# Optimization experiments

Hardware: AMD Instinct MI355X
Metric: run time of the kernel (lower is better)

The kernel has to match this reference:

```python
import jax, jax.numpy as jnp
import numpy as np

N = 50000   # nodes
E = 800000  # edges (avg degree 16)
D = 128     # in = hidden = out feats


def setup_inputs() -> dict:
    key = jax.random.key(0)
    ks = jax.random.split(key, 9)
    x = jax.random.normal(ks[0], (N, D), dtype=jnp.float32)
    edge_index = jax.random.randint(ks[1], (2, E), 0, N, dtype=jnp.int64)
    s = 1.0 / np.sqrt(D)
    # SAGEConv layer 0 (128 -> 128): lin_l (aggregated neighbors, with bias), lin_r (root, no bias)
    Wl0 = jax.random.uniform(ks[2], (D, D), jnp.float32, -s, s)
    Wr0 = jax.random.uniform(ks[3], (D, D), jnp.float32, -s, s)
    b0 = jax.random.uniform(ks[4], (D,), jnp.float32, -s, s)
    # SAGEConv layer 1 (128 -> 128)
    Wl1 = jax.random.uniform(ks[5], (D, D), jnp.float32, -s, s)
    Wr1 = jax.random.uniform(ks[6], (D, D), jnp.float32, -s, s)
    b1 = jax.random.uniform(ks[7], (D,), jnp.float32, -s, s)
    return {"x": x, "edge_index": edge_index,
            "Wl0": Wl0, "Wr0": Wr0, "b0": b0,
            "Wl1": Wl1, "Wr1": Wr1, "b1": b1}


def _sage_conv(x, src, dst, Wl, Wr, b):
    # mean aggregation of neighbor messages x[src] into dst nodes
    msgs = x[src]                                                    # [E, D]
    summed = jax.ops.segment_sum(msgs, dst, num_segments=N)         # [N, D]
    deg = jax.ops.segment_sum(jnp.ones((src.shape[0], 1), x.dtype), dst,
                              num_segments=N)                       # [N, 1]
    agg = summed / jnp.maximum(deg, 1.0)
    # out = lin_l(agg) + lin_r(x); only lin_l has bias (PyG default)
    return agg @ Wl.T + b + x @ Wr.T


def reference(x, edge_index, Wl0, Wr0, b0, Wl1, Wr1, b1):
    src, dst = edge_index[0], edge_index[1]
    h = jax.nn.relu(_sage_conv(x, src, dst, Wl0, Wr0, b0))
    out = _sage_conv(h, src, dst, Wl1, Wr1, b1)  # no ReLU on last layer
    return out
```

## Files before the change

### kernel.cpp

```cpp
#include <hip/hip_runtime.h>


#define D 128
#define NBITS 7
#define BNODES 128
#define GA 64
typedef unsigned short u16;
typedef unsigned u32;
typedef short bf16x8 __attribute__((ext_vector_type(8)));
typedef float f32x4 __attribute__((ext_vector_type(4)));

__device__ __forceinline__ u16 f2bf(float f) {
    union { float f; unsigned u; } x;
    x.f = f;
    unsigned r = x.u + 0x7FFF + ((x.u >> 16) & 1);
    return (u16)(r >> 16);
}
__device__ __forceinline__ float bf2f(u16 b) {
    union { unsigned u; float f; } x;
    x.u = ((unsigned)b) << 16;
    return x.f;
}

__global__ __launch_bounds__(1024) void hist_and_convert(
        const int* __restrict__ dst, int* __restrict__ Gcounts, int E, int NB, int chunk,
        const float* __restrict__ x, u16* __restrict__ xb, int xQuads,
        const float* __restrict__ w0, const float* __restrict__ w1,
        const float* __restrict__ w2, const float* __restrict__ w3,
        u16* __restrict__ o0, u16* __restrict__ o1,
        u16* __restrict__ o2, u16* __restrict__ o3) {
    if (blockIdx.x < GA) {
        __shared__ int cnt[512];
        for (int i = threadIdx.x; i < NB; i += 1024) cnt[i] = 0;
        __syncthreads();
        int base = blockIdx.x * chunk;
        int end = base + chunk; if (end > E) end = E;
        for (int e = base + threadIdx.x; e < end; e += 1024)
            atomicAdd(&cnt[dst[e] >> NBITS], 1);
        __syncthreads();
        for (int b = threadIdx.x; b < NB; b += 1024)
            Gcounts[b * GA + blockIdx.x] = cnt[b];
    } else {
        int i = (blockIdx.x - GA) * 1024 + threadIdx.x;
        if (i < xQuads) {
            float4 v = *(const float4*)&x[i * 4];
            ushort4 o;
            o.x = f2bf(v.x); o.y = f2bf(v.y); o.z = f2bf(v.z); o.w = f2bf(v.w);
            *(ushort4*)&xb[i * 4] = o;
        } else {
            int j = i - xQuads;
            const int q = D * D / 4;
            if (j < 4 * q) {
                int m = j / q, k = j % q;
                const float* in = (m == 0) ? w0 : (m == 1) ? w1 : (m == 2) ? w2 : w3;
                u16* op = (m == 0) ? o0 : (m == 1) ? o1 : (m == 2) ? o2 : o3;
                float4 v = *(const float4*)&in[k * 4];
                ushort4 o;
                o.x = f2bf(v.x); o.y = f2bf(v.y); o.z = f2bf(v.z); o.w = f2bf(v.w);
                *(ushort4*)&op[k * 4] = o;
            }
        }
    }
}

__global__ __launch_bounds__(1024) void scan1_kernel(const int* __restrict__ in,
                                                     int* __restrict__ excl,
                                                     int* __restrict__ totals, int n) {
    int chunk = blockIdx.x;
    int i = chunk * 1024 + threadIdx.x;
    int v = (i < n) ? in[i] : 0;
    int lane = threadIdx.x & 63;
    int wid = threadIdx.x >> 6;
    int s = v;
    #pragma unroll
    for (int off = 1; off < 64; off <<= 1) {
        int t = __shfl_up(s, off);
        if (lane >= off) s += t;
    }
    __shared__ int wsum[16];
    if (lane == 63) wsum[wid] = s;
    __syncthreads();
    if (wid == 0) {
        int ws = (lane < 16) ? wsum[lane] : 0;
        #pragma unroll
        for (int off = 1; off < 16; off <<= 1) {
            int t = __shfl_up(ws, off);
            if (lane >= off) ws += t;
        }
        if (lane < 16) wsum[lane] = ws;
    }
    __syncthreads();
    int wave_off = (wid > 0) ? wsum[wid - 1] : 0;
    int incl = s + wave_off;
    if (i < n) excl[i] = incl - v;
    if (threadIdx.x == 1023) totals[chunk] = incl;
}

__device__ __forceinline__ void load_choff(const int* __restrict__ totals,
                                           int nChunks, int* choff) {
    if (threadIdx.x < 64) {
        int t = threadIdx.x;
        int v = (t < nChunks) ? totals[t] : 0;
        int s = v;
        #pragma unroll
        for (int off = 1; off < 64; off <<= 1) {
            int u = __shfl_up(s, off);
            if (t >= off) s += u;
        }
        if (t < 32) choff[t] = s - v;
    }
}

__global__ __launch_bounds__(1024) void bucket_scatter(const int* __restrict__ src,
                                                       const int* __restrict__ dst,
                                                       const int* __restrict__ excl,
                                                       const int* __restrict__ totals,
                                                       u32* __restrict__ Ebuck,
                                                       int E, int NB, int chunk, int nChunks) {
    __shared__ int cur[512];
    __shared__ int choff[32];
    load_choff(totals, nChunks, choff);
    __syncthreads();
    for (int b = threadIdx.x; b < NB; b += 1024) {
        int idx = b * GA + blockIdx.x;
        cur[b] = excl[idx] + choff[idx >> 10];
    }
    __syncthreads();
    int base = blockIdx.x * chunk;
    int end = base + chunk; if (end > E) end = E;
    for (int e = base + threadIdx.x; e < end; e += 1024) {
        int d = dst[e];
        int b = d >> NBITS;
        int pos = atomicAdd(&cur[b], 1);
        Ebuck[pos] = ((u32)(d & (BNODES - 1)) << 16) | (u32)src[e];
    }
}

__global__ __launch_bounds__(256) void bucket_sort_csr(const u32* __restrict__ Ebuck,
                                                       const int* __restrict__ excl_g,
                                                       const int* __restrict__ totals,
                                                       int* __restrict__ row_ptr,
                                                       u16* __restrict__ csr,
                                                       int E, int N, int NB, int nChunks) {
    __shared__ int hist[BNODES], excl[BNODES], cur[BNODES];
    __shared__ u16 sorted[8192];
    __shared__ int choff[32];
    load_choff(totals, nChunks, choff);
    __syncthreads();
    int b = blockIdx.x;
    int idx0 = b * GA;
    int start = excl_g[idx0] + choff[idx0 >> 10];
    int endv = E;
    if (b + 1 < NB) {
        int idx1 = (b + 1) * GA;
        endv = excl_g[idx1] + choff[idx1 >> 10];
    }
    int cnt = endv - start;
    if (cnt > 8192) cnt = 8192;
    for (int i = threadIdx.x; i < BNODES; i += 256) hist[i] = 0;
    __syncthreads();
    for (int i = threadIdx.x; i < cnt; i += 256)
        atomicAdd(&hist[Ebuck[start + i] >> 16], 1);
    __syncthreads();
    if (threadIdx.x == 0) {
        int run = 0;
        for (int i = 0; i < BNODES; ++i) { excl[i] = run; run += hist[i]; }
    }
    __syncthreads();
    for (int i = threadIdx.x; i < BNODES; i += 256) {
        cur[i] = excl[i];
        int g = b * BNODES + i;
        if (g <= N) row_ptr[g] = start + excl[i];
    }
    __syncthreads();
    for (int i = threadIdx.x; i < cnt; i += 256) {
        u32 r = Ebuck[start + i];
        int pos = atomicAdd(&cur[r >> 16], 1);
        sorted[pos] = (u16)(r & 0xFFFF);
    }
    __syncthreads();
    for (int i = threadIdx.x; i < cnt; i += 256)
        csr[start + i] = sorted[i];
}

__global__ __launch_bounds__(256) void aggregate_bf16(const u16* __restrict__ xb,
                                                      const int* __restrict__ row_ptr,
                                                      const u16* __restrict__ csr,
                                                      u16* __restrict__ aggb, int n) {
    int node = blockIdx.x * 4 + (threadIdx.x >> 6);
    if (node >= n) return;
    int lane = threadIdx.x & 63;
    int half = lane >> 5;
    int fl = (lane & 31) * 4;
    int begin = row_ptr[node], end = row_ptr[node + 1];
    float a0 = 0.f, a1 = 0.f, a2 = 0.f, a3 = 0.f;
    int j = begin + half;
    for (; j + 2 < end; j += 4) {
        int s0 = csr[j], s1 = csr[j + 2];
        ushort4 v0 = *(const ushort4*)&xb[s0 * D + fl];
        ushort4 v1 = *(const ushort4*)&xb[s1 * D + fl];
        a0 += bf2f(v0.x) + bf2f(v1.x);
        a1 += bf2f(v0.y) + bf2f(v1.y);
        a2 += bf2f(v0.z) + bf2f(v1.z);
        a3 += bf2f(v0.w) + bf2f(v1.w);
    }
    if (j < end) {
        int s0 = csr[j];
        ushort4 v0 = *(const ushort4*)&xb[s0 * D + fl];
        a0 += bf2f(v0.x); a1 += bf2f(v0.y); a2 += bf2f(v0.z); a3 += bf2f(v0.w);
    }
    a0 += __shfl_xor(a0, 32);
    a1 += __shfl_xor(a1, 32);
    a2 += __shfl_xor(a2, 32);
    a3 += __shfl_xor(a3, 32);
    if (half == 0) {
        int d = end - begin;
        if (d < 1) d = 1;
        float inv = 1.0f / (float)d;
        ushort4 o;
        o.x = f2bf(a0 * inv); o.y = f2bf(a1 * inv);
        o.z = f2bf(a2 * inv); o.w = f2bf(a3 * inv);
        *(ushort4*)&aggb[node * D + fl] = o;
    }
}

#define LSTR 136

__global__ __launch_bounds__(256) void gemm_mfma(const u16* __restrict__ Aroot,
                                                 const u16* __restrict__ Wr,
                                                 const u16* __restrict__ Agg,
                                                 const u16* __restrict__ Wl,
                                                 const float* __restrict__ bias,
                                                 void* __restrict__ out,
                                                 int n, int mode) {
    __shared__ __align__(16) u16 Lr[64 * LSTR];
    __shared__ __align__(16) u16 Lg[64 * LSTR];
    const int tid = threadIdx.x;
    const int n0 = blockIdx.x * 64;

    {
        int row = tid >> 4;
        int c = (tid & 15) * 8;
        #pragma unroll
        for (int p = 0; p < 4; ++p) {
            int r = p * 16 + row;
            int g = n0 + r;
            float4 vr = make_float4(0.f, 0.f, 0.f, 0.f);
            float4 vg = make_float4(0.f, 0.f, 0.f, 0.f);
            if (g < n) {
                vr = *(const float4*)&Aroot[g * D + c];
                vg = *(const float4*)&Agg[g * D + c];
            }
            *(float4*)&Lr[r * LSTR + c] = vr;
            *(float4*)&Lg[r * LSTR + c] = vg;
        }
    }

    const int wave = tid >> 6;
    const int lane = tid & 63;
    const int quad = lane >> 4;
    const int l16 = lane & 15;

    bf16x8 wr[2][4], wl[2][4];
    #pragma unroll
    for (int mt = 0; mt < 2; ++mt) {
        int jrow = wave * 32 + mt * 16 + l16;
        #pragma unroll
        for (int kb = 0; kb < 4; ++kb) {
            wr[mt][kb] = *(const bf16x8*)&Wr[jrow * D + kb * 32 + quad * 8];
            wl[mt][kb] = *(const bf16x8*)&Wl[jrow * D + kb * 32 + quad * 8];
        }
    }

    __syncthreads();

    f32x4 acc[4][2];
    #pragma unroll
    for (int it = 0; it < 4; ++it)
        #pragma unroll
        for (int mt = 0; mt < 2; ++mt)
            acc[it][mt] = (f32x4){0.f, 0.f, 0.f, 0.f};

    #pragma unroll
    for (int it = 0; it < 4; ++it) {
        int base = (it * 16 + l16) * LSTR + quad * 8;
        #pragma unroll
        for (int kb = 0; kb < 4; ++kb) {
            bf16x8 bx = *(const bf16x8*)&Lr[base + kb * 32];
            bf16x8 bg = *(const bf16x8*)&Lg[base + kb * 32];
            #pragma unroll
            for (int mt = 0; mt < 2; ++mt) {
                acc[it][mt] = __builtin_amdgcn_mfma_f32_16x16x32_bf16(wr[mt][kb], bx, acc[it][mt], 0, 0, 0);
                acc[it][mt] = __builtin_amdgcn_mfma_f32_16x16x32_bf16(wl[mt][kb], bg, acc[it][mt], 0, 0, 0);
            }
        }
    }

    #pragma unroll
    for (int it = 0; it < 4; ++it) {
        int i = n0 + it * 16 + l16;
        if (i < n) {
            #pragma unroll
            for (int mt = 0; mt < 2; ++mt) {
                int j0 = wave * 32 + mt * 16 + quad * 4;
                float4 bv = *(const float4*)&bias[j0];
                float o0 = acc[it][mt][0] + bv.x;
                float o1 = acc[it][mt][1] + bv.y;
                float o2 = acc[it][mt][2] + bv.z;
                float o3 = acc[it][mt][3] + bv.w;
                if (mode) {
                    o0 = fmaxf(o0, 0.f); o1 = fmaxf(o1, 0.f);
                    o2 = fmaxf(o2, 0.f); o3 = fmaxf(o3, 0.f);
                    ushort4 ob;
                    ob.x = f2bf(o0); ob.y = f2bf(o1); ob.z = f2bf(o2); ob.w = f2bf(o3);
                    *(ushort4*)&((u16*)out)[i * D + j0] = ob;
                } else {
                    float4 of = make_float4(o0, o1, o2, o3);
                    *(float4*)&((float*)out)[i * D + j0] = of;
                }
            }
        }
    }
}


extern "C" void kernel_launch(void* const* d_in, const int* in_sizes, int n_in,
                              void* d_out, int out_size, void* d_ws, size_t ws_size,
                              hipStream_t stream) {
    const float* x = (const float*)d_in[0];
    const int* edge = (const int*)d_in[1];
    const float* Wl0 = (const float*)d_in[2];
    const float* Wr0 = (const float*)d_in[3];
    const float* b0 = (const float*)d_in[4];
    const float* Wl1 = (const float*)d_in[5];
    const float* Wr1 = (const float*)d_in[6];
    const float* b1 = (const float*)d_in[7];

    const int N = in_sizes[0] / D;
    const int E = in_sizes[1] / 2;
    const int* src = edge;
    const int* dst = edge + E;

    char* ws = (char*)d_ws;
    size_t off = 0;
    auto alloc = [&](size_t bytes) {
        char* p = ws + off;
        off += (bytes + 255) & ~(size_t)255;
        return p;
    };
    int* row_ptr = (int*)alloc((size_t)(N + 1) * 4);
    u32* Ebuck = (u32*)alloc((size_t)E * 4);
    u16* csrb = (u16*)alloc((size_t)E * 2);
    u16* xb = (u16*)alloc((size_t)N * D * 2);
    u16* hb = (u16*)alloc((size_t)N * D * 2);
    u16* aggb = (u16*)alloc((size_t)N * D * 2);
    u16* Wl0b = (u16*)alloc((size_t)D * D * 2);
    u16* Wr0b = (u16*)alloc((size_t)D * D * 2);
    u16* Wl1b = (u16*)alloc((size_t)D * D * 2);
    u16* Wr1b = (u16*)alloc((size_t)D * D * 2);
    const int NB = (N + BNODES - 1) / BNODES;
    const int scanN = NB * GA;
    int* Gcounts = (int*)alloc((size_t)scanN * 4);
    int* Sc = (int*)alloc((size_t)scanN * 4);
    int* totals = (int*)alloc(32 * 4);

    (void)ws_size; (void)n_in; (void)out_size;

    const int chunk = (E + GA - 1) / GA;
    const int xQuads = N * D / 4;
    const int convQuads = xQuads + 4 * D * D / 4;
    const int histGrid = GA + (convQuads + 1023) / 1024;
    const int nChunks = (scanN + 1023) / 1024;
    const int aggBlocks = (N + 3) / 4;
    const int gemmBlocks = (N + 63) / 64;

    hist_and_convert<<<histGrid, 1024, 0, stream>>>(
        dst, Gcounts, E, NB, chunk,
        x, xb, xQuads,
        Wl0, Wr0, Wl1, Wr1, Wl0b, Wr0b, Wl1b, Wr1b);
    scan1_kernel<<<nChunks, 1024, 0, stream>>>(Gcounts, Sc, totals, scanN);
    bucket_scatter<<<GA, 1024, 0, stream>>>(src, dst, Sc, totals, Ebuck, E, NB, chunk, nChunks);
    bucket_sort_csr<<<NB, 256, 0, stream>>>(Ebuck, Sc, totals, row_ptr, csrb, E, N, NB, nChunks);

    aggregate_bf16<<<aggBlocks, 256, 0, stream>>>(xb, row_ptr, csrb, aggb, N);
    gemm_mfma<<<gemmBlocks, 256, 0, stream>>>(xb, Wr0b, aggb, Wl0b, b0, hb, N, 1);
    aggregate_bf16<<<aggBlocks, 256, 0, stream>>>(hb, row_ptr, csrb, aggb, N);
    gemm_mfma<<<gemmBlocks, 256, 0, stream>>>(hb, Wr1b, aggb, Wl1b, b1, d_out, N, 0);
}
```

Baseline: 218.9 us.

## Store bf16 features in 32-wide column slabs for cache-local aggregation

Features, hidden activations and aggregates are stored as four slabs of 32 columns each instead of row-major 128 columns. Aggregation processes one slab per group of blocks so the gathered working set is a quarter of the full feature matrix and fits better in cache. In exchange the CSR indices and row pointers are read four times and each gather fetches only 64 bytes per row. The conversion kernel and GEMM loads and stores are adapted to the new layout.

```diff
diff --git a/kernel.cpp b/kernel.cpp
--- a/kernel.cpp
+++ b/kernel.cpp
@@ -24,7 +24,7 @@
 
 __global__ __launch_bounds__(1024) void hist_and_convert(
         const int* __restrict__ dst, int* __restrict__ Gcounts, int E, int NB, int chunk,
-        const float* __restrict__ x, u16* __restrict__ xb, int xQuads,
+        const float* __restrict__ x, u16* __restrict__ xq, int xOcts, int n32,
         const float* __restrict__ w0, const float* __restrict__ w1,
         const float* __restrict__ w2, const float* __restrict__ w3,
         u16* __restrict__ o0, u16* __restrict__ o1,
@@ -42,13 +42,20 @@
             Gcounts[b * GA + blockIdx.x] = cnt[b];
     } else {
         int i = (blockIdx.x - GA) * 1024 + threadIdx.x;
-        if (i < xQuads) {
-            float4 v = *(const float4*)&x[i * 4];
-            ushort4 o;
-            o.x = f2bf(v.x); o.y = f2bf(v.y); o.z = f2bf(v.z); o.w = f2bf(v.w);
-            *(ushort4*)&xb[i * 4] = o;
+        if (i < xOcts) {
+            int node = i >> 4;
+            int f = (i & 15) * 8;
+            int q = f >> 5, off = f & 31;
+            float4 va = *(const float4*)&x[node * D + f];
+            float4 vb = *(const float4*)&x[node * D + f + 4];
+            bf16x8 o;
+            o[0] = (short)f2bf(va.x); o[1] = (short)f2bf(va.y);
+            o[2] = (short)f2bf(va.z); o[3] = (short)f2bf(va.w);
+            o[4] = (short)f2bf(vb.x); o[5] = (short)f2bf(vb.y);
+            o[6] = (short)f2bf(vb.z); o[7] = (short)f2bf(vb.w);
+            *(bf16x8*)&xq[q * n32 + node * 32 + off] = o;
         } else {
-            int j = i - xQuads;
+            int j = i - xOcts;
             const int q = D * D / 4;
             if (j < 4 * q) {
                 int m = j / q, k = j % q;
@@ -183,44 +190,42 @@
         csr[start + i] = sorted[i];
 }
 
-__global__ __launch_bounds__(256) void aggregate_bf16(const u16* __restrict__ xb,
-                                                      const int* __restrict__ row_ptr,
-                                                      const u16* __restrict__ csr,
-                                                      u16* __restrict__ aggb, int n) {
-    int node = blockIdx.x * 4 + (threadIdx.x >> 6);
+__global__ __launch_bounds__(256) void aggregate_q(const u16* __restrict__ xq,
+                                                   const int* __restrict__ row_ptr,
+                                                   const u16* __restrict__ csr,
+                                                   u16* __restrict__ aggq,
+                                                   int n, int nb4, int n32) {
+    int bq = blockIdx.x / nb4;
+    int node = (blockIdx.x % nb4) * 4 + (threadIdx.x >> 6);
     if (node >= n) return;
     int lane = threadIdx.x & 63;
-    int half = lane >> 5;
-    int fl = (lane & 31) * 4;
+    int part = lane >> 4;
+    int fl = (lane & 15) * 2;
+    const u16* base = xq + bq * n32;
     int begin = row_ptr[node], end = row_ptr[node + 1];
-    float a0 = 0.f, a1 = 0.f, a2 = 0.f, a3 = 0.f;
-    int j = begin + half;
-    for (; j + 2 < end; j += 4) {
-        int s0 = csr[j], s1 = csr[j + 2];
-        ushort4 v0 = *(const ushort4*)&xb[s0 * D + fl];
-        ushort4 v1 = *(const ushort4*)&xb[s1 * D + fl];
-        a0 += bf2f(v0.x) + bf2f(v1.x);
-        a1 += bf2f(v0.y) + bf2f(v1.y);
-        a2 += bf2f(v0.z) + bf2f(v1.z);
-        a3 += bf2f(v0.w) + bf2f(v1.w);
-    }
-    if (j < end) {
+    float a0 = 0.f, a1 = 0.f;
+    int j = begin + part;
+    for (; j + 4 < end; j += 8) {
+        int s0 = csr[j], s1 = csr[j + 4];
+        u32 v0 = *(const u32*)&base[s0 * 32 + fl];
+        u32 v1 = *(const u32*)&base[s1 * 32 + fl];
+        a0 += bf2f((u16)v0) + bf2f((u16)v1);
+        a1 += bf2f((u16)(v0 >> 16)) + bf2f((u16)(v1 >> 16));
+    }
+    for (; j < end; j += 4) {
         int s0 = csr[j];
-        ushort4 v0 = *(const ushort4*)&xb[s0 * D + fl];
-        a0 += bf2f(v0.x); a1 += bf2f(v0.y); a2 += bf2f(v0.z); a3 += bf2f(v0.w);
-    }
-    a0 += __shfl_xor(a0, 32);
-    a1 += __shfl_xor(a1, 32);
-    a2 += __shfl_xor(a2, 32);
-    a3 += __shfl_xor(a3, 32);
-    if (half == 0) {
+        u32 v0 = *(const u32*)&base[s0 * 32 + fl];
+        a0 += bf2f((u16)v0);
+        a1 += bf2f((u16)(v0 >> 16));
+    }
+    a0 += __shfl_xor(a0, 16); a0 += __shfl_xor(a0, 32);
+    a1 += __shfl_xor(a1, 16); a1 += __shfl_xor(a1, 32);
+    if (part == 0) {
         int d = end - begin;
         if (d < 1) d = 1;
         float inv = 1.0f / (float)d;
-        ushort4 o;
-        o.x = f2bf(a0 * inv); o.y = f2bf(a1 * inv);
-        o.z = f2bf(a2 * inv); o.w = f2bf(a3 * inv);
-        *(ushort4*)&aggb[node * D + fl] = o;
+        u32 o = (u32)f2bf(a0 * inv) | ((u32)f2bf(a1 * inv) << 16);
+        *(u32*)&aggq[bq * n32 + node * 32 + fl] = o;
     }
 }
 
@@ -232,7 +237,7 @@
                                                  const u16* __restrict__ Wl,
                                                  const float* __restrict__ bias,
                                                  void* __restrict__ out,
-                                                 int n, int mode) {
+                                                 int n, int n32, int mode) {
     __shared__ __align__(16) u16 Lr[64 * LSTR];
     __shared__ __align__(16) u16 Lg[64 * LSTR];
     const int tid = threadIdx.x;
@@ -241,6 +246,9 @@
     {
         int row = tid >> 4;
         int c = (tid & 15) * 8;
+        int q = c >> 5, off = c & 31;
+        const u16* ar = Aroot + q * n32;
+        const u16* ag = Agg + q * n32;
         #pragma unroll
         for (int p = 0; p < 4; ++p) {
             int r = p * 16 + row;
@@ -248,8 +256,8 @@
             float4 vr = make_float4(0.f, 0.f, 0.f, 0.f);
             float4 vg = make_float4(0.f, 0.f, 0.f, 0.f);
             if (g < n) {
-                vr = *(const float4*)&Aroot[g * D + c];
-                vg = *(const float4*)&Agg[g * D + c];
+                vr = *(const float4*)&ar[g * 32 + off];
+                vg = *(const float4*)&ag[g * 32 + off];
             }
             *(float4*)&Lr[r * LSTR + c] = vr;
             *(float4*)&Lg[r * LSTR + c] = vg;
@@ -313,7 +321,8 @@
                     o2 = fmaxf(o2, 0.f); o3 = fmaxf(o3, 0.f);
                     ushort4 ob;
                     ob.x = f2bf(o0); ob.y = f2bf(o1); ob.z = f2bf(o2); ob.w = f2bf(o3);
-                    *(ushort4*)&((u16*)out)[i * D + j0] = ob;
+                    int jj = mt * 16 + quad * 4;
+                    *(ushort4*)&((u16*)out)[wave * n32 + i * 32 + jj] = ob;
                 } else {
                     float4 of = make_float4(o0, o1, o2, o3);
                     *(float4*)&((float*)out)[i * D + j0] = of;
@@ -351,9 +360,9 @@
     int* row_ptr = (int*)alloc((size_t)(N + 1) * 4);
     u32* Ebuck = (u32*)alloc((size_t)E * 4);
     u16* csrb = (u16*)alloc((size_t)E * 2);
-    u16* xb = (u16*)alloc((size_t)N * D * 2);
-    u16* hb = (u16*)alloc((size_t)N * D * 2);
-    u16* aggb = (u16*)alloc((size_t)N * D * 2);
+    u16* xq = (u16*)alloc((size_t)N * D * 2);
+    u16* hq = (u16*)alloc((size_t)N * D * 2);
+    u16* aggq = (u16*)alloc((size_t)N * D * 2);
     u16* Wl0b = (u16*)alloc((size_t)D * D * 2);
     u16* Wr0b = (u16*)alloc((size_t)D * D * 2);
     u16* Wl1b = (u16*)alloc((size_t)D * D * 2);
@@ -367,23 +376,25 @@
     (void)ws_size; (void)n_in; (void)out_size;
 
     const int chunk = (E + GA - 1) / GA;
-    const int xQuads = N * D / 4;
-    const int convQuads = xQuads + 4 * D * D / 4;
-    const int histGrid = GA + (convQuads + 1023) / 1024;
+    const int n32 = N * 32;
+    const int xOcts = N * D / 8;
+    const int convThreads = xOcts + 4 * D * D / 4;
+    const int histGrid = GA + (convThreads + 1023) / 1024;
     const int nChunks = (scanN + 1023) / 1024;
-    const int aggBlocks = (N + 3) / 4;
+    const int nb4 = (N + 3) / 4;
+    const int aggBlocks = 4 * nb4;
     const int gemmBlocks = (N + 63) / 64;
 
     hist_and_convert<<<histGrid, 1024, 0, stream>>>(
         dst, Gcounts, E, NB, chunk,
-        x, xb, xQuads,
+        x, xq, xOcts, n32,
         Wl0, Wr0, Wl1, Wr1, Wl0b, Wr0b, Wl1b, Wr1b);
     scan1_kernel<<<nChunks, 1024, 0, stream>>>(Gcounts, Sc, totals, scanN);
     bucket_scatter<<<GA, 1024, 0, stream>>>(src, dst, Sc, totals, Ebuck, E, NB, chunk, nChunks);
     bucket_sort_csr<<<NB, 256, 0, stream>>>(Ebuck, Sc, totals, row_ptr, csrb, E, N, NB, nChunks);
 
-    aggregate_bf16<<<aggBlocks, 256, 0, stream>>>(xb, row_ptr, csrb, aggb, N);
-    gemm_mfma<<<gemmBlocks, 256, 0, stream>>>(xb, Wr0b, aggb, Wl0b, b0, hb, N, 1);
-    aggregate_bf16<<<aggBlocks, 256, 0, stream>>>(hb, row_ptr, csrb, aggb, N);
-    gemm_mfma<<<gemmBlocks, 256, 0, stream>>>(hb, Wr1b, aggb, Wl1b, b1, d_out, N, 0);
-}
+    aggregate_q<<<aggBlocks, 256, 0, stream>>>(xq, row_ptr, csrb, aggq, N, nb4, n32);
+    gemm_mfma<<<gemmBlocks, 256, 0, stream>>>(xq, Wr0b, aggq, Wl0b, b0, hq, N, n32, 1);
+    aggregate_q<<<aggBlocks, 256, 0, stream>>>(hq, row_ptr, csrb, aggq, N, nb4, n32);
+    gemm_mfma<<<gemmBlocks, 256, 0, stream>>>(hq, Wr1b, aggq, Wl1b, b1, d_out, N, n32, 0);
+}
```

After: 290.1 us. 32.5% more time.
